# Performance work log

Measured on AMD Instinct MI355X. Metric: run time of the kernel, lower is better.

## Reference

```python
import jax, jax.numpy as jnp
import numpy as np
from jax import lax

S, B, F, H = 2048, 512, 1, 128  # seq_len, minibatch, feature_count, mlp hidden


def setup_inputs() -> dict:
    key = jax.random.key(0)
    ks = jax.random.split(key, 7)
    x = jax.random.normal(ks[0], (S, B, F), dtype=jnp.float32)
    # derivative network: 2 -> H -> H -> 2 tanh MLP (ignores t, as in repo)
    W1 = jax.random.normal(ks[1], (2, H), dtype=jnp.float32) / np.sqrt(2.0)
    b1 = jnp.zeros((H,), dtype=jnp.float32)
    W2 = jax.random.normal(ks[2], (H, H), dtype=jnp.float32) / np.sqrt(H)
    b2 = jnp.zeros((H,), dtype=jnp.float32)
    W3 = jax.random.normal(ks[3], (H, 2), dtype=jnp.float32) / np.sqrt(H)
    b3 = jnp.zeros((2,), dtype=jnp.float32)
    return {"x": x, "W1": W1, "b1": b1, "W2": W2, "b2": b2, "W3": W3, "b3": b3}


def reference(x, W1, b1, W2, b2, W3, b3):
    # x: (S, B, 1). Per step n: v = [x_n, state] in R^2 per sequence,
    # one forward-Euler step with dt = (n) - (n-1) = 1.0:
    #   y1 = v + dt * f(v)
    # output_n = y1[..., 1]; state <- output_n. Strict sequential recurrence.
    def mlp(v):  # v: (B, 2)
        h = jnp.tanh(v @ W1 + b1)
        h = jnp.tanh(h @ W2 + b2)
        return h @ W3 + b3  # (B, 2)

    dt = jnp.float32(1.0)

    def step(state, x_n):  # state: (B,1), x_n: (B,1)
        v = jnp.concatenate([x_n, state], axis=1)  # (B, 2)
        y1 = v + dt * mlp(v)
        out = y1[:, 1:2]  # channel 1 of the 2-dim ODE state
        return out, out

    init = jnp.zeros((x.shape[1], 1), dtype=x.dtype)
    _, ys = lax.scan(step, init, x)  # (S, B, 1)
    return ys
```

## Files before the change

### kernel.cpp

```cpp
#include <hip/hip_runtime.h>

#define SEQ 2048
#define BATCH 512
#define HDIM 128

typedef __bf16 bf16x8 __attribute__((ext_vector_type(8)));
typedef float  f32x4  __attribute__((ext_vector_type(4)));
typedef unsigned int uint32;

__device__ __forceinline__ float tanh_e2(float y) {
    float e;
    asm("v_exp_f32 %0, %1" : "=v"(e) : "v"(y));
    return fmaf(-2.0f, __builtin_amdgcn_rcpf(e + 1.0f), 1.0f);
}

template<int CTRL>
__device__ __forceinline__ float dpp_add(float x) {
    return x + __int_as_float(__builtin_amdgcn_update_dpp(
        0, __float_as_int(x), CTRL, 0xf, 0xf, true));
}

__global__ __launch_bounds__(512, 4)
void odenet_scan_kernel(const float* __restrict__ x,
                        const float* __restrict__ W1,
                        const float* __restrict__ b1,
                        const float* __restrict__ W2,
                        const float* __restrict__ b2,
                        const float* __restrict__ W3,
                        const float* __restrict__ b3,
                        float* __restrict__ out)
{
    const int t  = threadIdx.x;
    const int l  = t & 63;
    const int wv = t >> 6;
    const int b  = blockIdx.x;

    constexpr float CS = 2.8853900817779268f;

    __shared__ float xbuf[SEQ];
    __shared__ unsigned short hbuf[2][144];
    __shared__ __align__(16) float ybuf[8];

    #pragma unroll
    for (int i = 0; i < 4; ++i)
        xbuf[i * 512 + t] = x[(i * 512 + t) * BATCH + b];

    bf16x8 Bhi[4], Blo[4];
    const int bc = 16 * wv + (l & 15);
    #pragma unroll
    for (int kt = 0; kt < 4; ++kt) {
        union { unsigned short u[8]; bf16x8 v; } fh, fl;
        #pragma unroll
        for (int j = 0; j < 8; ++j) {
            const int k = 32 * kt + 8 * (l >> 4) + j;
            const float v = W2[k * HDIM + bc] * CS;
            const uint32 u = __float_as_uint(v);
            fh.u[j] = (unsigned short)(u >> 16);
            const float hif = __uint_as_float(u & 0xffff0000u);
            fl.u[j] = (unsigned short)(__float_as_uint(v - hif) >> 16);
        }
        Bhi[kt] = fh.v;
        Blo[kt] = fl.v;
    }

    const float b2v = b2[bc] * CS;
    const float w3v = W3[2 * bc + 1];
    const float b31 = b3[1];

    float w1xv = 0.0f, w1sv = 0.0f, b1vv = 0.0f;
    if (t < 128) {
        w1xv = W1[t] * CS;
        w1sv = W1[HDIM + t] * CS;
        b1vv = b1[t] * CS;
    }

    const int rowe = ((l & 15) == 0) ? 0 : 1;
    const unsigned short* pA = &hbuf[rowe][8 * (l >> 4)];

    __syncthreads();

    float s = 0.0f, s_hold = 0.0f;

    if (t < 128) {
        const float h = tanh_e2(fmaf(w1xv, xbuf[0], b1vv));
        const uint32 u = __float_as_uint(h);
        hbuf[0][t] = (unsigned short)(u >> 16);
        const float hf = __uint_as_float(u & 0xffff0000u);
        hbuf[1][t] = (unsigned short)(__float_as_uint(h - hf) >> 16);
    }
    __syncthreads();

    for (int n = 0; n < SEQ; ++n) {
        float pre1 = 0.0f;
        if (t < 128)
            pre1 = fmaf(w1xv, xbuf[(n + 1) & (SEQ - 1)], b1vv);

        f32x4 Ch = {0.0f, 0.0f, 0.0f, 0.0f};
        f32x4 Cl = {0.0f, 0.0f, 0.0f, 0.0f};
        #pragma unroll
        for (int kt = 0; kt < 4; ++kt) {
            const bf16x8 a = __builtin_bit_cast(bf16x8,
                *reinterpret_cast<const uint4*>(pA + 32 * kt));
            Ch = __builtin_amdgcn_mfma_f32_16x16x32_bf16(a, Bhi[kt], Ch, 0, 0, 0);
            Cl = __builtin_amdgcn_mfma_f32_16x16x32_bf16(a, Blo[kt], Cl, 0, 0, 0);
        }
        const float p = (Ch[0] + Ch[1]) + (Cl[0] + b2v);
        float z = tanh_e2(p) * w3v;
        z = dpp_add<0xB1>(z);
        z = dpp_add<0x4E>(z);
        z = dpp_add<0x141>(z);
        z = dpp_add<0x140>(z);
        if (l == 0) ybuf[wv] = z;
        __syncthreads();

        if (t < 128) {
            const float4 y0 = *reinterpret_cast<const float4*>(&ybuf[0]);
            const float4 y1 = *reinterpret_cast<const float4*>(&ybuf[4]);
            s += ((y0.x + y0.y) + (y0.z + y0.w))
               + ((y1.x + y1.y) + (y1.z + y1.w)) + b31;

            if (t < 64) {
                if (l == (n & 63)) s_hold = s;
                if ((n & 63) == 63) out[(n - 63 + l) * BATCH + b] = s_hold;
            }

            const float h = tanh_e2(fmaf(w1sv, s, pre1));
            const uint32 u = __float_as_uint(h);
            hbuf[0][t] = (unsigned short)(u >> 16);
            const float hf = __uint_as_float(u & 0xffff0000u);
            hbuf[1][t] = (unsigned short)(__float_as_uint(h - hf) >> 16);
        }
        __syncthreads();
    }
}

extern "C" void kernel_launch(void* const* d_in, const int* in_sizes, int n_in,
                              void* d_out, int out_size, void* d_ws, size_t ws_size,
                              hipStream_t stream) {
    const float* x  = (const float*)d_in[0];
    const float* W1 = (const float*)d_in[1];
    const float* b1 = (const float*)d_in[2];
    const float* W2 = (const float*)d_in[3];
    const float* b2 = (const float*)d_in[4];
    const float* W3 = (const float*)d_in[5];
    const float* b3 = (const float*)d_in[6];
    float* out = (float*)d_out;

    dim3 grid(BATCH);
    dim3 block(512);
    odenet_scan_kernel<<<grid, block, 0, stream>>>(x, W1, b1, W2, b2, W3, b3, out);
}
```

Before: 988.0 us.

## Process two batch sequences per block using spare MFMA rows

Each block now handles two independent sequences instead of one. Hidden states for both are packed into the 16-row MFMA A operand: rows 0-1 carry the hi/lo bf16 split for sequence A and rows 2-3 for sequence B. The grid is halved, and the per-step MFMA, sync and reduction costs are shared across two sequences. The price is extra tanh and DPP work per step, twice as many threads in the layer-1 section, and fewer resident blocks per CU from the lowered launch bound, so the per-step critical path gets longer.

Measured after the change: 1.120 ms. 13.4% more time.

```diff
diff --git a/kernel.cpp b/kernel.cpp
--- a/kernel.cpp
+++ b/kernel.cpp
@@ -20,7 +20,7 @@
         0, __float_as_int(x), CTRL, 0xf, 0xf, true));
 }
 
-__global__ __launch_bounds__(512, 4)
+__global__ __launch_bounds__(512, 2)
 void odenet_scan_kernel(const float* __restrict__ x,
                         const float* __restrict__ W1,
                         const float* __restrict__ b1,
@@ -33,17 +33,17 @@
     const int t  = threadIdx.x;
     const int l  = t & 63;
     const int wv = t >> 6;
-    const int b  = blockIdx.x;
+    const int b0 = 2 * blockIdx.x;
 
     constexpr float CS = 2.8853900817779268f;
 
-    __shared__ float xbuf[SEQ];
-    __shared__ unsigned short hbuf[2][144];
-    __shared__ __align__(16) float ybuf[8];
+    __shared__ float2 xbuf[SEQ];
+    __shared__ unsigned short hbuf[4 * 144];
+    __shared__ __align__(16) float2 ybuf[8];
 
     #pragma unroll
     for (int i = 0; i < 4; ++i)
-        xbuf[i * 512 + t] = x[(i * 512 + t) * BATCH + b];
+        xbuf[i * 512 + t] = *reinterpret_cast<const float2*>(&x[(i * 512 + t) * BATCH + b0]);
 
     bf16x8 Bhi[4], Blo[4];
     const int bc = 16 * wv + (l & 15);
@@ -67,33 +67,39 @@
     const float w3v = W3[2 * bc + 1];
     const float b31 = b3[1];
 
+    const int hcol = t & 127;
+    const int hch  = t >> 7;
     float w1xv = 0.0f, w1sv = 0.0f, b1vv = 0.0f;
-    if (t < 128) {
-        w1xv = W1[t] * CS;
-        w1sv = W1[HDIM + t] * CS;
-        b1vv = b1[t] * CS;
+    if (t < 256) {
+        w1xv = W1[hcol] * CS;
+        w1sv = W1[HDIM + hcol] * CS;
+        b1vv = b1[hcol] * CS;
     }
+    unsigned short* pWhi = &hbuf[(2 * hch + 0) * 144 + hcol];
+    unsigned short* pWlo = &hbuf[(2 * hch + 1) * 144 + hcol];
 
-    const int rowe = ((l & 15) == 0) ? 0 : 1;
-    const unsigned short* pA = &hbuf[rowe][8 * (l >> 4)];
+    const unsigned short* pA = &hbuf[(l & 3) * 144 + 8 * (l >> 4)];
 
     __syncthreads();
 
     float s = 0.0f, s_hold = 0.0f;
 
-    if (t < 128) {
-        const float h = tanh_e2(fmaf(w1xv, xbuf[0], b1vv));
+    if (t < 256) {
+        const float2 x0 = xbuf[0];
+        const float h = tanh_e2(fmaf(w1xv, hch ? x0.y : x0.x, b1vv));
         const uint32 u = __float_as_uint(h);
-        hbuf[0][t] = (unsigned short)(u >> 16);
+        *pWhi = (unsigned short)(u >> 16);
         const float hf = __uint_as_float(u & 0xffff0000u);
-        hbuf[1][t] = (unsigned short)(__float_as_uint(h - hf) >> 16);
+        *pWlo = (unsigned short)(__float_as_uint(h - hf) >> 16);
     }
     __syncthreads();
 
     for (int n = 0; n < SEQ; ++n) {
         float pre1 = 0.0f;
-        if (t < 128)
-            pre1 = fmaf(w1xv, xbuf[(n + 1) & (SEQ - 1)], b1vv);
+        if (t < 256) {
+            const float2 xn2 = xbuf[(n + 1) & (SEQ - 1)];
+            pre1 = fmaf(w1xv, hch ? xn2.y : xn2.x, b1vv);
+        }
 
         f32x4 Ch = {0.0f, 0.0f, 0.0f, 0.0f};
         f32x4 Cl = {0.0f, 0.0f, 0.0f, 0.0f};
@@ -104,31 +110,36 @@
             Ch = __builtin_amdgcn_mfma_f32_16x16x32_bf16(a, Bhi[kt], Ch, 0, 0, 0);
             Cl = __builtin_amdgcn_mfma_f32_16x16x32_bf16(a, Blo[kt], Cl, 0, 0, 0);
         }
-        const float p = (Ch[0] + Ch[1]) + (Cl[0] + b2v);
-        float z = tanh_e2(p) * w3v;
-        z = dpp_add<0xB1>(z);
-        z = dpp_add<0x4E>(z);
-        z = dpp_add<0x141>(z);
-        z = dpp_add<0x140>(z);
-        if (l == 0) ybuf[wv] = z;
+        const float pAv = (Ch[0] + Ch[1]) + (Cl[0] + b2v);
+        const float pBv = (Ch[2] + Ch[3]) + (Cl[2] + b2v);
+        float zA = tanh_e2(pAv) * w3v;
+        float zB = tanh_e2(pBv) * w3v;
+        zA = dpp_add<0xB1>(zA);   zB = dpp_add<0xB1>(zB);
+        zA = dpp_add<0x4E>(zA);   zB = dpp_add<0x4E>(zB);
+        zA = dpp_add<0x141>(zA);  zB = dpp_add<0x141>(zB);
+        zA = dpp_add<0x140>(zA);  zB = dpp_add<0x140>(zB);
+        if (l == 0) ybuf[wv] = make_float2(zA, zB);
         __syncthreads();
 
-        if (t < 128) {
-            const float4 y0 = *reinterpret_cast<const float4*>(&ybuf[0]);
-            const float4 y1 = *reinterpret_cast<const float4*>(&ybuf[4]);
-            s += ((y0.x + y0.y) + (y0.z + y0.w))
-               + ((y1.x + y1.y) + (y1.z + y1.w)) + b31;
+        if (t < 256) {
+            const float4* yq = reinterpret_cast<const float4*>(&ybuf[0]);
+            const float4 q0 = yq[0], q1 = yq[1], q2 = yq[2], q3 = yq[3];
+            const float dyA = ((q0.x + q0.z) + (q1.x + q1.z))
+                            + ((q2.x + q2.z) + (q3.x + q3.z)) + b31;
+            const float dyB = ((q0.y + q0.w) + (q1.y + q1.w))
+                            + ((q2.y + q2.w) + (q3.y + q3.w)) + b31;
+            s += hch ? dyB : dyA;
 
-            if (t < 64) {
+            if ((t & 127) < 64) {
                 if (l == (n & 63)) s_hold = s;
-                if ((n & 63) == 63) out[(n - 63 + l) * BATCH + b] = s_hold;
+                if ((n & 63) == 63) out[(n - 63 + l) * BATCH + b0 + hch] = s_hold;
             }
 
             const float h = tanh_e2(fmaf(w1sv, s, pre1));
             const uint32 u = __float_as_uint(h);
-            hbuf[0][t] = (unsigned short)(u >> 16);
+            *pWhi = (unsigned short)(u >> 16);
             const float hf = __uint_as_float(u & 0xffff0000u);
-            hbuf[1][t] = (unsigned short)(__float_as_uint(h - hf) >> 16);
+            *pWlo = (unsigned short)(__float_as_uint(h - hf) >> 16);
         }
         __syncthreads();
     }
@@ -146,7 +157,7 @@
     const float* b3 = (const float*)d_in[6];
     float* out = (float*)d_out;
 
-    dim3 grid(BATCH);
+    dim3 grid(BATCH / 2);
     dim3 block(512);
     odenet_scan_kernel<<<grid, block, 0, stream>>>(x, W1, b1, W2, b2, W3, b3, out);
 }
```
